# Performance work log

Hardware: AMD Instinct MI355X
Metric: run time of the kernel (lower is better)

Reference implementation:

```python
import jax, jax.numpy as jnp
import numpy as np
from jax import lax

FEAT_STRIDE = 16
SCALES = np.array([8, 16, 32], dtype=np.float64)
RATIOS = np.array([0.5, 1, 2], dtype=np.float64)
PRE_NMS_TOP_N = 6000
POST_NMS_TOP_N = 1000
NMS_THRESH = 0.7

# ---- anchor generation (numpy, static constants) ----

def _whctrs(a):
    w = a[2] - a[0] + 1.0
    h = a[3] - a[1] + 1.0
    return w, h, a[0] + 0.5 * (w - 1.0), a[1] + 0.5 * (h - 1.0)

def _mkanchors(ws, hs, xc, yc):
    return np.stack([xc - 0.5 * (ws - 1.0), yc - 0.5 * (hs - 1.0),
                     xc + 0.5 * (ws - 1.0), yc + 0.5 * (hs - 1.0)], axis=1)

def _ratio_enum(anchor, ratios):
    w, h, xc, yc = _whctrs(anchor)
    size = w * h
    ws = np.round(np.sqrt(size / ratios))
    hs = np.round(ws * ratios)
    return _mkanchors(ws, hs, xc, yc)

def _scale_enum(anchor, scales):
    w, h, xc, yc = _whctrs(anchor)
    return _mkanchors(w * scales, h * scales, xc, yc)

def generate_anchors(base_size=16):
    base = np.array([1, 1, base_size, base_size], dtype=np.float64) - 1.0
    ra = _ratio_enum(base, RATIOS)
    return np.vstack([_scale_enum(ra[i], SCALES) for i in range(ra.shape[0])]).astype(np.float32)


def setup_inputs() -> dict:
    key = jax.random.key(0)
    k1, k2 = jax.random.split(key)
    H, W, A = 76, 128, 9
    scores = jax.random.uniform(k1, (1, 2 * A, H, W), dtype=jnp.float32)
    bbox_delta = jax.random.normal(k2, (1, 4 * A, H, W), dtype=jnp.float32) * 0.1
    im_info = jnp.array([H * FEAT_STRIDE, W * FEAT_STRIDE, 1.0], dtype=jnp.float32)  # [h, w, scale]
    return {"scores": scores, "bbox_delta": bbox_delta, "im_info": im_info}


def reference(scores, bbox_delta, im_info):
    anchors = generate_anchors()            # [A, 4]
    A = anchors.shape[0]
    H, W = scores.shape[2], scores.shape[3]

    # grid of shifted anchors: [K*A, 4], anchor index varies fastest (matches permute layout)
    sx = np.arange(W) * FEAT_STRIDE
    sy = np.arange(H) * FEAT_STRIDE
    sx, sy = np.meshgrid(sx, sy)
    shifts = np.stack([sx.ravel(), sy.ravel(), sx.ravel(), sy.ravel()], axis=1).astype(np.float32)  # [K,4]
    all_anchors = jnp.asarray((anchors[None, :, :] + shifts[:, None, :]).reshape(-1, 4))  # [K*A,4]

    # foreground scores, NHWC flatten -> [K*A]
    fg = jnp.transpose(scores[0, A:], (1, 2, 0)).reshape(-1)
    # deltas, NHWC flatten -> [K*A, 4]
    deltas = jnp.transpose(bbox_delta[0], (1, 2, 0)).reshape(-1, 4)

    aw = all_anchors[:, 2] - all_anchors[:, 0] + 1.0
    ah = all_anchors[:, 3] - all_anchors[:, 1] + 1.0
    acx = all_anchors[:, 0] + 0.5 * aw
    acy = all_anchors[:, 1] + 0.5 * ah
    pcx = deltas[:, 0] * aw + acx
    pcy = deltas[:, 1] * ah + acy
    pw = jnp.exp(deltas[:, 2]) * aw
    ph = jnp.exp(deltas[:, 3]) * ah
    boxes = jnp.stack([pcx - 0.5 * pw, pcy - 0.5 * ph, pcx + 0.5 * pw, pcy + 0.5 * ph], axis=1)

    # clip_boxes to image
    xmax = im_info[1] - 1.0
    ymax = im_info[0] - 1.0
    boxes = jnp.stack([jnp.clip(boxes[:, 0], 0.0, xmax), jnp.clip(boxes[:, 1], 0.0, ymax),
                       jnp.clip(boxes[:, 2], 0.0, xmax), jnp.clip(boxes[:, 3], 0.0, ymax)], axis=1)

    # pre-NMS top-N by fg score
    top_scores, top_idx = lax.top_k(fg, PRE_NMS_TOP_N)
    props = boxes[top_idx]                  # [N, 4], sorted by score desc

    # pairwise IoU (+1 convention)
    x1, y1, x2, y2 = props[:, 0], props[:, 1], props[:, 2], props[:, 3]
    areas = (x2 - x1 + 1.0) * (y2 - y1 + 1.0)
    iw = jnp.clip(jnp.minimum(x2[:, None], x2[None, :]) - jnp.maximum(x1[:, None], x1[None, :]) + 1.0, 0.0)
    ih = jnp.clip(jnp.minimum(y2[:, None], y2[None, :]) - jnp.maximum(y1[:, None], y1[None, :]) + 1.0, 0.0)
    inter = iw * ih
    iou = inter / (areas[:, None] + areas[None, :] - inter)  # [N, N]

    # sequential greedy NMS over score-sorted boxes
    N = PRE_NMS_TOP_N
    later = jnp.arange(N)
    def body(i, keep):
        sup = (iou[i] > NMS_THRESH) & keep[i] & (later > i)
        return keep & ~sup
    keep = lax.fori_loop(0, N, body, jnp.ones((N,), dtype=bool))

    masked = jnp.where(keep, top_scores, -jnp.inf)
    _, sel = lax.top_k(masked, POST_NMS_TOP_N)
    return props[sel]                       # [POST_NMS_TOP_N, 4]
```

## Files before the change

### kernel.cpp

```cpp
#include <hip/hip_runtime.h>
#include <cstdint>

#define HH 76
#define WW 128
#define AA 9
#define HWH (HH * WW)
#define KK (HWH * AA)
#define NSEL 6000
#define NCH 94
#define NPAD (NCH * 64)
#define NOUT 1000
#define NMS_T 0.7
#define NTRI (NCH * (NCH + 1) / 2)
#define MASK_BLOCKS 1117
#define SELCAP 16384
#define BINCAP 2048
#define NBIN 16384

#define LBAR() asm volatile("s_waitcnt lgkmcnt(0)\n\ts_barrier" ::: "memory")

#define WS_HIST 0
#define WS_BINB 65536
#define WS_NACT 65540
#define WS_ACTIVE 65552
#define WS_BINSTART 98320
#define WS_SELKEYS 163856
#define WS_BOXES 294928
#define WS_MASK 391184

__device__ __constant__ float c_ax1[9] = {-84.f, -176.f, -360.f, -56.f, -120.f, -248.f, -36.f, -80.f, -168.f};
__device__ __constant__ float c_ay1[9] = {-40.f, -88.f, -184.f, -56.f, -120.f, -248.f, -80.f, -168.f, -344.f};
__device__ __constant__ float c_ax2[9] = {99.f, 191.f, 375.f, 71.f, 135.f, 263.f, 51.f, 95.f, 183.f};
__device__ __constant__ float c_ay2[9] = {55.f, 103.f, 199.f, 71.f, 135.f, 263.f, 95.f, 183.f, 359.f};

__device__ __forceinline__ unsigned score_key(float s) {
    unsigned u = __float_as_uint(s);
    return (u & 0x80000000u) ? ~u : (u | 0x80000000u);
}

__device__ __forceinline__ int key_bin(unsigned key) {
    int bi = (int)(key >> 16) - 0x8000;
    return bi < 0 ? 0 : (bi > NBIN - 1 ? NBIN - 1 : bi);
}

__device__ __forceinline__ unsigned long long chunk_scan_fix(unsigned long long col,
                                                             unsigned long long alive_in) {
    unsigned long long kept = alive_in;
    while (true) {
        unsigned long long sup = __ballot((int)((col & kept) != 0ull));
        unsigned long long kept2 = alive_in & ~sup;
        if (kept2 == kept) return kept;
        kept = kept2;
    }
}

__global__ __launch_bounds__(1024) void k_front1(const float* __restrict__ scores,
                                                 unsigned* __restrict__ histG,
                                                 unsigned* __restrict__ binB,
                                                 unsigned* __restrict__ binStart,
                                                 unsigned* __restrict__ activeList,
                                                 unsigned* __restrict__ nact,
                                                 unsigned long long* __restrict__ selKeys) {
    __shared__ unsigned hloc[NBIN];
    __shared__ unsigned seg[1024];
    __shared__ unsigned Bsh;
    int t = threadIdx.x;
    if (t == 0) *nact = 0;
#pragma unroll
    for (int k = 0; k < NBIN / 1024; ++k) hloc[t + k * 1024] = 0;
    __syncthreads();
    for (int g = t; g < KK / 4; g += 1024) {
        float4 v = ((const float4*)(scores + AA * HWH))[g];
        atomicAdd(&hloc[key_bin(score_key(v.x))], 1u);
        atomicAdd(&hloc[key_bin(score_key(v.y))], 1u);
        atomicAdd(&hloc[key_bin(score_key(v.z))], 1u);
        atomicAdd(&hloc[key_bin(score_key(v.w))], 1u);
    }
    __syncthreads();

    unsigned local[16];
    unsigned ssum = 0;
#pragma unroll
    for (int k = 0; k < 16; ++k) { local[k] = hloc[t * 16 + k]; ssum += local[k]; }
    seg[t] = ssum;
    __syncthreads();
    for (int off = 1; off < 1024; off <<= 1) {
        unsigned v = seg[t];
        unsigned add = (t + off < 1024) ? seg[t + off] : 0u;
        __syncthreads();
        seg[t] = v + add;
        __syncthreads();
    }
    unsigned above = (t + 1 < 1024) ? seg[t + 1] : 0u;
    if (above < NSEL && above + ssum >= NSEL) {
        unsigned acc = above;
#pragma unroll
        for (int b = 15; b >= 0; --b) {
            acc += local[b];
            if (acc >= NSEL) { Bsh = (unsigned)(t * 16 + b); *binB = Bsh; break; }
        }
    }
    __syncthreads();
    unsigned B = Bsh;
    if ((unsigned)(t * 16 + 15) >= B) {
        unsigned acc2 = above;
        for (int k = 15; k >= 0; --k) {
            unsigned bin = (unsigned)(t * 16 + k);
            if (bin < B) break;
            if (local[k] > 0) {
                binStart[bin] = acc2;
                histG[bin] = local[k];
                hloc[bin] = acc2;
                unsigned tick = atomicAdd(nact, 1u);
                if (tick < 8192) activeList[tick] = bin;
            }
            acc2 += local[k];
        }
    }
    __syncthreads();

    for (int g = t; g < KK / 4; g += 1024) {
        float4 v = ((const float4*)(scores + AA * HWH))[g];
        float sv[4] = {v.x, v.y, v.z, v.w};
#pragma unroll
        for (int k = 0; k < 4; ++k) {
            int j = g * 4 + k;
            unsigned key = score_key(sv[k]);
            unsigned bin = (unsigned)key_bin(key);
            if (bin >= B) {
                int a = j / HWH;
                int hw = j - a * HWH;
                unsigned i = (unsigned)(hw * AA + a);
                unsigned pos = atomicAdd(&hloc[bin], 1u);
                if (pos < SELCAP)
                    selKeys[pos] = ((unsigned long long)key << 32) | (unsigned)(~i);
            }
        }
    }
}

__global__ __launch_bounds__(256) void k_binsort(const unsigned* __restrict__ histG,
                                                 const unsigned* __restrict__ binStart,
                                                 const unsigned* __restrict__ activeList,
                                                 const unsigned* __restrict__ nact,
                                                 unsigned long long* __restrict__ selKeys,
                                                 const float* __restrict__ bbox,
                                                 const float* __restrict__ im_info,
                                                 float4* __restrict__ boxes) {
    __shared__ unsigned long long sk[BINCAP];
    int t = threadIdx.x;
    unsigned na = *nact;
    if (na > 8192) na = 8192;
    double xmax = (double)im_info[1] - 1.0, ymax = (double)im_info[0] - 1.0;
    for (unsigned aIdx = blockIdx.x; aIdx < na; aIdx += gridDim.x) {
        unsigned bin = activeList[aIdx];
        unsigned ntot = histG[bin];
        unsigned base = binStart[bin];
        unsigned n = ntot > BINCAP ? BINCAP : ntot;
        unsigned m = 64; while (m < n) m <<= 1;
        for (unsigned p = t; p < m; p += 256) sk[p] = (p < n) ? selKeys[base + p] : 0ull;
        __syncthreads();
        for (unsigned size = 2; size <= m; size <<= 1) {
            for (unsigned stride = size >> 1; stride > 0; stride >>= 1) {
                for (unsigned p = (unsigned)t; p < m / 2; p += 256) {
                    unsigned i = 2u * p - (p & (stride - 1u));
                    unsigned j = i + stride;
                    bool up = (i & size) != 0;
                    unsigned long long a = sk[i], b = sk[j];
                    bool doswap = up ? (a > b) : (a < b);
                    if (doswap) { sk[i] = b; sk[j] = a; }
                }
                __syncthreads();
            }
        }
        for (unsigned r = t; r < n; r += 256) {
            unsigned g = base + r;
            if (g >= NSEL) continue;
            unsigned i = ~(unsigned)(sk[r] & 0xFFFFFFFFull);
            int a = (int)(i % AA);
            int hw = (int)(i / AA);
            int h = hw >> 7, w = hw & 127;
            double sx = 16.0 * w, sy = 16.0 * h;
            double ax1 = (double)c_ax1[a] + sx, ay1 = (double)c_ay1[a] + sy;
            double ax2 = (double)c_ax2[a] + sx, ay2 = (double)c_ay2[a] + sy;
            double aw = ax2 - ax1 + 1.0, ah = ay2 - ay1 + 1.0;
            double acx = ax1 + 0.5 * aw, acy = ay1 + 0.5 * ah;
            int bse = h * WW + w;
            double d0 = (double)bbox[(4 * a + 0) * HWH + bse];
            double d1 = (double)bbox[(4 * a + 1) * HWH + bse];
            double d2 = (double)bbox[(4 * a + 2) * HWH + bse];
            double d3 = (double)bbox[(4 * a + 3) * HWH + bse];
            double pcx = d0 * aw + acx, pcy = d1 * ah + acy;
            double pw = exp(d2) * aw, ph = exp(d3) * ah;
            double x1 = fmin(fmax(pcx - 0.5 * pw, 0.0), xmax);
            double y1 = fmin(fmax(pcy - 0.5 * ph, 0.0), ymax);
            double x2 = fmin(fmax(pcx + 0.5 * pw, 0.0), xmax);
            double y2 = fmin(fmax(pcy + 0.5 * ph, 0.0), ymax);
            boxes[g] = make_float4((float)x1, (float)y1, (float)x2, (float)y2);
        }
        __syncthreads();
    }
}

__global__ __launch_bounds__(256) void k_mask(const float4* __restrict__ boxes,
                                              unsigned long long* __restrict__ supT) {
    __shared__ float4 cb[4][64];
    int wave = threadIdx.x >> 6, lane = threadIdx.x & 63;
    for (int L = blockIdx.x * 4 + wave; L < NTRI; L += MASK_BLOCKS * 4) {
        int rc = 0, rem = L;
        while (rem >= NCH - rc) { rem -= NCH - rc; rc++; }
        int cc = rc + rem;
        cb[wave][lane] = boxes[cc * 64 + lane];
        int gi = rc * 64 + lane;
        unsigned long long bits = 0ull;
        if (gi < NSEL) {
            float4 rb = boxes[gi];
            double rx1 = rb.x, ry1 = rb.y, rx2 = rb.z, ry2 = rb.w;
            double rarea = (rx2 - rx1 + 1.0) * (ry2 - ry1 + 1.0);
            for (int j = 0; j < 64; ++j) {
                int gj = cc * 64 + j;
                float4 c = cb[wave][j];
                double iw = fmin(rx2, (double)c.z) - fmax(rx1, (double)c.x) + 1.0;
                double ih = fmin(ry2, (double)c.w) - fmax(ry1, (double)c.y) + 1.0;
                if (gj > gi && gj < NSEL && iw > 0.0 && ih > 0.0) {
                    double inter = iw * ih;
                    double carea = ((double)c.z - (double)c.x + 1.0) * ((double)c.w - (double)c.y + 1.0);
                    double uni = rarea + carea - inter;
                    if (inter > NMS_T * uni) bits |= (1ull << j);
                }
            }
        }
        unsigned long long myword = 0ull;
        for (int j = 0; j < 64; ++j) {
            unsigned long long bal = __ballot((int)((bits >> j) & 1ull));
            if (lane == j) myword = bal;
        }
        supT[(size_t)rc * NPAD + cc * 64 + lane] = myword;
    }
}

__global__ __launch_bounds__(512, 1) void k_nms(const unsigned long long* __restrict__ supT,
                                                const float4* __restrict__ boxes,
                                                float4* __restrict__ out) {
    __shared__ unsigned long long colLds[NCH][64];
    __shared__ unsigned long long removed[NCH];
    __shared__ unsigned long long aliveArr[NCH];
    __shared__ int cstop;
    __shared__ unsigned scanBuf[8];
    int t = threadIdx.x;
    int wave = t >> 6, lane = t & 63;

    for (int c = wave; c < NCH; c += 8)
        colLds[c][lane] = supT[(size_t)c * NPAD + c * 64 + lane];
    for (int i = t; i < NCH; i += 512) removed[i] = (i == NCH - 1) ? 0xFFFF000000000000ull : 0ull;
    if (t == 0) cstop = -1;
    __syncthreads();
    if (wave == 0) __builtin_amdgcn_s_setprio(1);

    unsigned long long wAA = 0, wAB = 0;
    unsigned long long mA[8], mB[8];
#pragma unroll
    for (int q = 0; q < 8; ++q) { mA[q] = 0; mB[q] = 0; }
    if (wave == 0) wAA = supT[(size_t)0 * NPAD + 1 * 64 + lane];
    unsigned keptTot = 0;

    for (int c = 0; c < NCH; c += 2) {
        if (wave == 0) {
            if (c + 2 < NCH) wAB = supT[(size_t)(c + 1) * NPAD + (c + 2) * 64 + lane];
            unsigned long long alive_in = ~removed[c];
            unsigned long long alive = chunk_scan_fix(colLds[c][lane], alive_in);
            keptTot += (unsigned)__popcll(alive);
            if (lane == 0) {
                removed[c] = ~alive;
                aliveArr[c] = alive;
                if (keptTot >= NOUT) cstop = c;
            }
            if (c + 1 < NCH) {
                unsigned long long ball = __ballot((int)((wAA & alive) != 0ull));
                if (lane == 0 && ball) atomicOr(&removed[c + 1], ball);
            }
        } else {
            if (c + 2 < NCH) {
#pragma unroll
                for (int q = 0; q < 8; ++q) {
                    int cp = (wave - 1) + 7 * q;
                    mB[q] = (cp < c + 1) ? supT[(size_t)cp * NPAD + (c + 2) * 64 + lane] : 0ull;
                }
            }
            if (c + 1 < NCH) {
                unsigned long long acc = 0ull;
#pragma unroll
                for (int q = 0; q < 8; ++q) {
                    int cp = (wave - 1) + 7 * q;
                    if (cp < c) acc |= __ballot((int)((mA[q] & aliveArr[cp]) != 0ull));
                }
                for (int cp = (wave - 1) + 56; cp < c; cp += 7) {
                    unsigned long long wv = supT[(size_t)cp * NPAD + (c + 1) * 64 + lane];
                    acc |= __ballot((int)((wv & aliveArr[cp]) != 0ull));
                }
                if (lane == 0 && acc) atomicOr(&removed[c + 1], acc);
            }
        }
        LBAR();
        if (cstop >= 0) break;
        if (c + 1 >= NCH) break;

        if (wave == 0) {
            if (c + 3 < NCH) wAA = supT[(size_t)(c + 2) * NPAD + (c + 3) * 64 + lane];
            unsigned long long alive_in = ~removed[c + 1];
            unsigned long long alive = chunk_scan_fix(colLds[c + 1][lane], alive_in);
            keptTot += (unsigned)__popcll(alive);
            if (lane == 0) {
                removed[c + 1] = ~alive;
                aliveArr[c + 1] = alive;
                if (keptTot >= NOUT) cstop = c + 1;
            }
            if (c + 2 < NCH) {
                unsigned long long ball = __ballot((int)((wAB & alive) != 0ull));
                if (lane == 0 && ball) atomicOr(&removed[c + 2], ball);
            }
        } else {
            if (c + 3 < NCH) {
#pragma unroll
                for (int q = 0; q < 8; ++q) {
                    int cp = (wave - 1) + 7 * q;
                    mA[q] = (cp < c + 2) ? supT[(size_t)cp * NPAD + (c + 3) * 64 + lane] : 0ull;
                }
            }
            if (c + 2 < NCH) {
                unsigned long long acc = 0ull;
#pragma unroll
                for (int q = 0; q < 8; ++q) {
                    int cp = (wave - 1) + 7 * q;
                    if (cp < c + 1) acc |= __ballot((int)((mB[q] & aliveArr[cp]) != 0ull));
                }
                for (int cp = (wave - 1) + 56; cp < c + 1; cp += 7) {
                    unsigned long long wv = supT[(size_t)cp * NPAD + (c + 2) * 64 + lane];
                    acc |= __ballot((int)((wv & aliveArr[cp]) != 0ull));
                }
                if (lane == 0 && acc) atomicOr(&removed[c + 2], acc);
            }
        }
        LBAR();
        if (cstop >= 0) break;
    }
    if (wave == 0) __builtin_amdgcn_s_setprio(0);
    __syncthreads();

    int base = t * 12;
    unsigned cnt = 0, keepbits = 0;
    for (int q = 0; q < 12; ++q) {
        int i = base + q;
        if (i < NSEL) {
            bool kp = !((removed[i >> 6] >> (i & 63)) & 1ull);
            if (kp) { cnt++; keepbits |= (1u << q); }
        }
    }
    unsigned v = cnt;
#pragma unroll
    for (int off = 1; off < 64; off <<= 1) {
        unsigned u = (unsigned)__shfl_up((int)v, off, 64);
        if (lane >= off) v += u;
    }
    if (lane == 63) scanBuf[wave] = v;
    __syncthreads();
    unsigned waveOff = 0, NK = 0;
#pragma unroll
    for (int ww = 0; ww < 8; ++ww) {
        unsigned wv = scanBuf[ww];
        if (ww < wave) waveOff += wv;
        NK += wv;
    }
    unsigned incl = waveOff + v;
    unsigned kpos = incl - cnt;
    for (int q = 0; q < 12; ++q) {
        int i = base + q;
        if (i < NSEL) {
            bool kp = (keepbits >> q) & 1u;
            unsigned pos = kp ? kpos : (NK + (unsigned)i - kpos);
            if (kp) kpos++;
            if (pos < NOUT) out[pos] = boxes[i];
        }
    }
}

extern "C" void kernel_launch(void* const* d_in, const int* in_sizes, int n_in,
                              void* d_out, int out_size, void* d_ws, size_t ws_size,
                              hipStream_t stream) {
    const float* scores = (const float*)d_in[0];
    const float* bbox = (const float*)d_in[1];
    const float* im_info = (const float*)d_in[2];
    char* ws = (char*)d_ws;

    unsigned* histG = (unsigned*)(ws + WS_HIST);
    unsigned* binB = (unsigned*)(ws + WS_BINB);
    unsigned* nact = (unsigned*)(ws + WS_NACT);
    unsigned* activeList = (unsigned*)(ws + WS_ACTIVE);
    unsigned* binStart = (unsigned*)(ws + WS_BINSTART);
    unsigned long long* selKeys = (unsigned long long*)(ws + WS_SELKEYS);
    float4* boxes = (float4*)(ws + WS_BOXES);
    unsigned long long* supT = (unsigned long long*)(ws + WS_MASK);
    float4* out = (float4*)d_out;

    k_front1<<<1, 1024, 0, stream>>>(scores, histG, binB, binStart, activeList, nact, selKeys);
    k_binsort<<<64, 256, 0, stream>>>(histG, binStart, activeList, nact, selKeys, bbox, im_info, boxes);
    k_mask<<<MASK_BLOCKS, 256, 0, stream>>>(boxes, supT);
    k_nms<<<1, 512, 0, stream>>>(supT, boxes, out);
}
```

Measured before the change: 97.85 us.

## Fuse bin-sort and IoU mask kernels with a grid-wide atomic barrier

Merges the per-bin sort and box-decode kernel with the pairwise suppression-mask kernel into a single launch. The first 64 blocks sort bins and write boxes, then signal an atomic counter, and every block spins until that counter reaches 64 before computing mask tiles. This removes one kernel launch and its inter-kernel gap. In exchange it relies on all blocks being co-resident, and the larger shared buffer may lower occupancy in the mask phase.

```diff
diff --git a/kernel.cpp b/kernel.cpp
--- a/kernel.cpp
+++ b/kernel.cpp
@@ -12,7 +12,8 @@
 #define NOUT 1000
 #define NMS_T 0.7
 #define NTRI (NCH * (NCH + 1) / 2)
-#define MASK_BLOCKS 1117
+#define SM_BLOCKS 1117
+#define SORT_BLOCKS 64
 #define SELCAP 16384
 #define BINCAP 2048
 #define NBIN 16384
@@ -22,6 +23,7 @@
 #define WS_HIST 0
 #define WS_BINB 65536
 #define WS_NACT 65540
+#define WS_DONE 65544
 #define WS_ACTIVE 65552
 #define WS_BINSTART 98320
 #define WS_SELKEYS 163856
@@ -60,12 +62,13 @@
                                                  unsigned* __restrict__ binStart,
                                                  unsigned* __restrict__ activeList,
                                                  unsigned* __restrict__ nact,
+                                                 unsigned* __restrict__ doneCtr,
                                                  unsigned long long* __restrict__ selKeys) {
     __shared__ unsigned hloc[NBIN];
     __shared__ unsigned seg[1024];
     __shared__ unsigned Bsh;
     int t = threadIdx.x;
-    if (t == 0) *nact = 0;
+    if (t == 0) { *nact = 0; *doneCtr = 0; }
 #pragma unroll
     for (int k = 0; k < NBIN / 1024; ++k) hloc[t + k * 1024] = 0;
     __syncthreads();
@@ -139,78 +142,92 @@
     }
 }
 
-__global__ __launch_bounds__(256) void k_binsort(const unsigned* __restrict__ histG,
-                                                 const unsigned* __restrict__ binStart,
-                                                 const unsigned* __restrict__ activeList,
-                                                 const unsigned* __restrict__ nact,
-                                                 unsigned long long* __restrict__ selKeys,
-                                                 const float* __restrict__ bbox,
-                                                 const float* __restrict__ im_info,
-                                                 float4* __restrict__ boxes) {
-    __shared__ unsigned long long sk[BINCAP];
+__global__ __launch_bounds__(256) void k_sortmask(const unsigned* __restrict__ histG,
+                                                  const unsigned* __restrict__ binStart,
+                                                  const unsigned* __restrict__ activeList,
+                                                  const unsigned* __restrict__ nact,
+                                                  unsigned long long* __restrict__ selKeys,
+                                                  const float* __restrict__ bbox,
+                                                  const float* __restrict__ im_info,
+                                                  float4* __restrict__ boxes,
+                                                  unsigned* __restrict__ doneCtr,
+                                                  unsigned long long* __restrict__ supT) {
+    __shared__ __align__(16) unsigned long long shm[BINCAP];
     int t = threadIdx.x;
-    unsigned na = *nact;
-    if (na > 8192) na = 8192;
-    double xmax = (double)im_info[1] - 1.0, ymax = (double)im_info[0] - 1.0;
-    for (unsigned aIdx = blockIdx.x; aIdx < na; aIdx += gridDim.x) {
-        unsigned bin = activeList[aIdx];
-        unsigned ntot = histG[bin];
-        unsigned base = binStart[bin];
-        unsigned n = ntot > BINCAP ? BINCAP : ntot;
-        unsigned m = 64; while (m < n) m <<= 1;
-        for (unsigned p = t; p < m; p += 256) sk[p] = (p < n) ? selKeys[base + p] : 0ull;
+
+    if (blockIdx.x < SORT_BLOCKS) {
+        unsigned long long* sk = shm;
+        unsigned na = *nact;
+        if (na > 8192) na = 8192;
+        double xmax = (double)im_info[1] - 1.0, ymax = (double)im_info[0] - 1.0;
+        for (unsigned aIdx = blockIdx.x; aIdx < na; aIdx += SORT_BLOCKS) {
+            unsigned bin = activeList[aIdx];
+            unsigned ntot = histG[bin];
+            unsigned base = binStart[bin];
+            unsigned n = ntot > BINCAP ? BINCAP : ntot;
+            unsigned m = 64; while (m < n) m <<= 1;
+            for (unsigned p = t; p < m; p += 256) sk[p] = (p < n) ? selKeys[base + p] : 0ull;
+            __syncthreads();
+            for (unsigned size = 2; size <= m; size <<= 1) {
+                for (unsigned stride = size >> 1; stride > 0; stride >>= 1) {
+                    for (unsigned p = (unsigned)t; p < m / 2; p += 256) {
+                        unsigned i = 2u * p - (p & (stride - 1u));
+                        unsigned j = i + stride;
+                        bool up = (i & size) != 0;
+                        unsigned long long a = sk[i], b = sk[j];
+                        bool doswap = up ? (a > b) : (a < b);
+                        if (doswap) { sk[i] = b; sk[j] = a; }
+                    }
+                    __syncthreads();
+                }
+            }
+            for (unsigned r = t; r < n; r += 256) {
+                unsigned g = base + r;
+                if (g >= NSEL) continue;
+                unsigned i = ~(unsigned)(sk[r] & 0xFFFFFFFFull);
+                int a = (int)(i % AA);
+                int hw = (int)(i / AA);
+                int h = hw >> 7, w = hw & 127;
+                double sx = 16.0 * w, sy = 16.0 * h;
+                double ax1 = (double)c_ax1[a] + sx, ay1 = (double)c_ay1[a] + sy;
+                double ax2 = (double)c_ax2[a] + sx, ay2 = (double)c_ay2[a] + sy;
+                double aw = ax2 - ax1 + 1.0, ah = ay2 - ay1 + 1.0;
+                double acx = ax1 + 0.5 * aw, acy = ay1 + 0.5 * ah;
+                int bse = h * WW + w;
+                double d0 = (double)bbox[(4 * a + 0) * HWH + bse];
+                double d1 = (double)bbox[(4 * a + 1) * HWH + bse];
+                double d2 = (double)bbox[(4 * a + 2) * HWH + bse];
+                double d3 = (double)bbox[(4 * a + 3) * HWH + bse];
+                double pcx = d0 * aw + acx, pcy = d1 * ah + acy;
+                double pw = exp(d2) * aw, ph = exp(d3) * ah;
+                double x1 = fmin(fmax(pcx - 0.5 * pw, 0.0), xmax);
+                double y1 = fmin(fmax(pcy - 0.5 * ph, 0.0), ymax);
+                double x2 = fmin(fmax(pcx + 0.5 * pw, 0.0), xmax);
+                double y2 = fmin(fmax(pcy + 0.5 * ph, 0.0), ymax);
+                boxes[g] = make_float4((float)x1, (float)y1, (float)x2, (float)y2);
+            }
+            __syncthreads();
+        }
+        __threadfence();
         __syncthreads();
-        for (unsigned size = 2; size <= m; size <<= 1) {
-            for (unsigned stride = size >> 1; stride > 0; stride >>= 1) {
-                for (unsigned p = (unsigned)t; p < m / 2; p += 256) {
-                    unsigned i = 2u * p - (p & (stride - 1u));
-                    unsigned j = i + stride;
-                    bool up = (i & size) != 0;
-                    unsigned long long a = sk[i], b = sk[j];
-                    bool doswap = up ? (a > b) : (a < b);
-                    if (doswap) { sk[i] = b; sk[j] = a; }
-                }
-                __syncthreads();
-            }
-        }
-        for (unsigned r = t; r < n; r += 256) {
-            unsigned g = base + r;
-            if (g >= NSEL) continue;
-            unsigned i = ~(unsigned)(sk[r] & 0xFFFFFFFFull);
-            int a = (int)(i % AA);
-            int hw = (int)(i / AA);
-            int h = hw >> 7, w = hw & 127;
-            double sx = 16.0 * w, sy = 16.0 * h;
-            double ax1 = (double)c_ax1[a] + sx, ay1 = (double)c_ay1[a] + sy;
-            double ax2 = (double)c_ax2[a] + sx, ay2 = (double)c_ay2[a] + sy;
-            double aw = ax2 - ax1 + 1.0, ah = ay2 - ay1 + 1.0;
-            double acx = ax1 + 0.5 * aw, acy = ay1 + 0.5 * ah;
-            int bse = h * WW + w;
-            double d0 = (double)bbox[(4 * a + 0) * HWH + bse];
-            double d1 = (double)bbox[(4 * a + 1) * HWH + bse];
-            double d2 = (double)bbox[(4 * a + 2) * HWH + bse];
-            double d3 = (double)bbox[(4 * a + 3) * HWH + bse];
-            double pcx = d0 * aw + acx, pcy = d1 * ah + acy;
-            double pw = exp(d2) * aw, ph = exp(d3) * ah;
-            double x1 = fmin(fmax(pcx - 0.5 * pw, 0.0), xmax);
-            double y1 = fmin(fmax(pcy - 0.5 * ph, 0.0), ymax);
-            double x2 = fmin(fmax(pcx + 0.5 * pw, 0.0), xmax);
-            double y2 = fmin(fmax(pcy + 0.5 * ph, 0.0), ymax);
-            boxes[g] = make_float4((float)x1, (float)y1, (float)x2, (float)y2);
-        }
-        __syncthreads();
-    }
-}
-
-__global__ __launch_bounds__(256) void k_mask(const float4* __restrict__ boxes,
-                                              unsigned long long* __restrict__ supT) {
-    __shared__ float4 cb[4][64];
-    int wave = threadIdx.x >> 6, lane = threadIdx.x & 63;
-    for (int L = blockIdx.x * 4 + wave; L < NTRI; L += MASK_BLOCKS * 4) {
+        if (t == 0) __hip_atomic_fetch_add(doneCtr, 1u, __ATOMIC_ACQ_REL, __HIP_MEMORY_SCOPE_AGENT);
+    }
+
+    if (t == 0) {
+        while (__hip_atomic_load(doneCtr, __ATOMIC_ACQUIRE, __HIP_MEMORY_SCOPE_AGENT) <
+               (unsigned)SORT_BLOCKS)
+            __builtin_amdgcn_s_sleep(1);
+    }
+    __syncthreads();
+    __threadfence();
+
+    float4* cb = (float4*)shm;
+    int wave = t >> 6, lane = t & 63;
+    for (int L = blockIdx.x * 4 + wave; L < NTRI; L += SM_BLOCKS * 4) {
         int rc = 0, rem = L;
         while (rem >= NCH - rc) { rem -= NCH - rc; rc++; }
         int cc = rc + rem;
-        cb[wave][lane] = boxes[cc * 64 + lane];
+        cb[wave * 64 + lane] = boxes[cc * 64 + lane];
         int gi = rc * 64 + lane;
         unsigned long long bits = 0ull;
         if (gi < NSEL) {
@@ -219,7 +236,7 @@
             double rarea = (rx2 - rx1 + 1.0) * (ry2 - ry1 + 1.0);
             for (int j = 0; j < 64; ++j) {
                 int gj = cc * 64 + j;
-                float4 c = cb[wave][j];
+                float4 c = cb[wave * 64 + j];
                 double iw = fmin(rx2, (double)c.z) - fmax(rx1, (double)c.x) + 1.0;
                 double ih = fmin(ry2, (double)c.w) - fmax(ry1, (double)c.y) + 1.0;
                 if (gj > gi && gj < NSEL && iw > 0.0 && ih > 0.0) {
@@ -395,6 +412,7 @@
     unsigned* histG = (unsigned*)(ws + WS_HIST);
     unsigned* binB = (unsigned*)(ws + WS_BINB);
     unsigned* nact = (unsigned*)(ws + WS_NACT);
+    unsigned* doneCtr = (unsigned*)(ws + WS_DONE);
     unsigned* activeList = (unsigned*)(ws + WS_ACTIVE);
     unsigned* binStart = (unsigned*)(ws + WS_BINSTART);
     unsigned long long* selKeys = (unsigned long long*)(ws + WS_SELKEYS);
@@ -402,8 +420,8 @@
     unsigned long long* supT = (unsigned long long*)(ws + WS_MASK);
     float4* out = (float4*)d_out;
 
-    k_front1<<<1, 1024, 0, stream>>>(scores, histG, binB, binStart, activeList, nact, selKeys);
-    k_binsort<<<64, 256, 0, stream>>>(histG, binStart, activeList, nact, selKeys, bbox, im_info, boxes);
-    k_mask<<<MASK_BLOCKS, 256, 0, stream>>>(boxes, supT);
+    k_front1<<<1, 1024, 0, stream>>>(scores, histG, binB, binStart, activeList, nact, doneCtr, selKeys);
+    k_sortmask<<<SM_BLOCKS, 256, 0, stream>>>(histG, binStart, activeList, nact, selKeys,
+                                              bbox, im_info, boxes, doneCtr, supT);
     k_nms<<<1, 512, 0, stream>>>(supT, boxes, out);
 }
```

New measurement: 260.6 us. +166.4%, slower.

## Fuse per-bin sort and box decode into front kernel using rank sort

Applied to the files above, without the earlier changes.

Removes the separate k_binsort launch and runs the per-bin sorting and box decoding inside the single-block k_front1 kernel. Each of the 16 waves takes bins in turn and places every key by rank counting in LDS instead of a bitonic sort. Bins larger than 512 entries are deferred to a block-wide rank-sort pass. This saves a kernel launch and the bitonic barrier rounds, but all of the decode and sort work now runs on one workgroup instead of 64 blocks.

```diff
diff --git a/kernel.cpp b/kernel.cpp
--- a/kernel.cpp
+++ b/kernel.cpp
@@ -14,7 +14,6 @@
 #define NTRI (NCH * (NCH + 1) / 2)
 #define MASK_BLOCKS 1117
 #define SELCAP 16384
-#define BINCAP 2048
 #define NBIN 16384
 
 #define LBAR() asm volatile("s_waitcnt lgkmcnt(0)\n\ts_barrier" ::: "memory")
@@ -54,18 +53,49 @@
     }
 }
 
+__device__ __forceinline__ void decode_box(unsigned i, double xmax, double ymax,
+                                           const float* __restrict__ bbox,
+                                           float4* __restrict__ boxes, unsigned g) {
+    int a = (int)(i % AA);
+    int hw = (int)(i / AA);
+    int h = hw >> 7, w = hw & 127;
+    double sx = 16.0 * w, sy = 16.0 * h;
+    double ax1 = (double)c_ax1[a] + sx, ay1 = (double)c_ay1[a] + sy;
+    double ax2 = (double)c_ax2[a] + sx, ay2 = (double)c_ay2[a] + sy;
+    double aw = ax2 - ax1 + 1.0, ah = ay2 - ay1 + 1.0;
+    double acx = ax1 + 0.5 * aw, acy = ay1 + 0.5 * ah;
+    int bse = h * WW + w;
+    double d0 = (double)bbox[(4 * a + 0) * HWH + bse];
+    double d1 = (double)bbox[(4 * a + 1) * HWH + bse];
+    double d2 = (double)bbox[(4 * a + 2) * HWH + bse];
+    double d3 = (double)bbox[(4 * a + 3) * HWH + bse];
+    double pcx = d0 * aw + acx, pcy = d1 * ah + acy;
+    double pw = exp(d2) * aw, ph = exp(d3) * ah;
+    double x1 = fmin(fmax(pcx - 0.5 * pw, 0.0), xmax);
+    double y1 = fmin(fmax(pcy - 0.5 * ph, 0.0), ymax);
+    double x2 = fmin(fmax(pcx + 0.5 * pw, 0.0), xmax);
+    double y2 = fmin(fmax(pcy + 0.5 * ph, 0.0), ymax);
+    boxes[g] = make_float4((float)x1, (float)y1, (float)x2, (float)y2);
+}
+
 __global__ __launch_bounds__(1024) void k_front1(const float* __restrict__ scores,
+                                                 const float* __restrict__ bbox,
+                                                 const float* __restrict__ im_info,
                                                  unsigned* __restrict__ histG,
                                                  unsigned* __restrict__ binB,
                                                  unsigned* __restrict__ binStart,
                                                  unsigned* __restrict__ activeList,
                                                  unsigned* __restrict__ nact,
-                                                 unsigned long long* __restrict__ selKeys) {
-    __shared__ unsigned hloc[NBIN];
-    __shared__ unsigned seg[1024];
+                                                 unsigned long long* __restrict__ selKeys,
+                                                 float4* __restrict__ boxes) {
+    __shared__ __align__(16) unsigned char smemBuf[NBIN * 4 + 4096];
     __shared__ unsigned Bsh;
+    __shared__ unsigned bigList[64];
+    __shared__ unsigned nbig;
+    unsigned* hloc = (unsigned*)smemBuf;
+    unsigned* seg = (unsigned*)(smemBuf + NBIN * 4);
     int t = threadIdx.x;
-    if (t == 0) *nact = 0;
+    if (t == 0) { *nact = 0; nbig = 0; }
 #pragma unroll
     for (int k = 0; k < NBIN / 1024; ++k) hloc[t + k * 1024] = 0;
     __syncthreads();
@@ -137,66 +167,52 @@
             }
         }
     }
-}
-
-__global__ __launch_bounds__(256) void k_binsort(const unsigned* __restrict__ histG,
-                                                 const unsigned* __restrict__ binStart,
-                                                 const unsigned* __restrict__ activeList,
-                                                 const unsigned* __restrict__ nact,
-                                                 unsigned long long* __restrict__ selKeys,
-                                                 const float* __restrict__ bbox,
-                                                 const float* __restrict__ im_info,
-                                                 float4* __restrict__ boxes) {
-    __shared__ unsigned long long sk[BINCAP];
-    int t = threadIdx.x;
+    __syncthreads();
+
+    double xmax = (double)im_info[1] - 1.0, ymax = (double)im_info[0] - 1.0;
     unsigned na = *nact;
     if (na > 8192) na = 8192;
-    double xmax = (double)im_info[1] - 1.0, ymax = (double)im_info[0] - 1.0;
-    for (unsigned aIdx = blockIdx.x; aIdx < na; aIdx += gridDim.x) {
+    int wave = t >> 6, lane = t & 63;
+    unsigned long long* skbAll = (unsigned long long*)smemBuf;
+    unsigned long long* skb = skbAll + wave * 512;
+    for (unsigned aIdx = (unsigned)wave; aIdx < na; aIdx += 16) {
         unsigned bin = activeList[aIdx];
-        unsigned ntot = histG[bin];
+        unsigned n = histG[bin];
         unsigned base = binStart[bin];
-        unsigned n = ntot > BINCAP ? BINCAP : ntot;
-        unsigned m = 64; while (m < n) m <<= 1;
-        for (unsigned p = t; p < m; p += 256) sk[p] = (p < n) ? selKeys[base + p] : 0ull;
+        if (n > 512) {
+            if (lane == 0) {
+                unsigned p = atomicAdd(&nbig, 1u);
+                if (p < 64) bigList[p] = aIdx;
+            }
+            continue;
+        }
+        for (unsigned p = lane; p < n; p += 64) skb[p] = selKeys[base + p];
+        asm volatile("s_waitcnt lgkmcnt(0)" ::: "memory");
+        for (unsigned r = lane; r < n; r += 64) {
+            unsigned long long key = skb[r];
+            unsigned rank = 0;
+            for (unsigned j = 0; j < n; ++j) rank += (skb[j] > key) ? 1u : 0u;
+            unsigned g = base + rank;
+            if (g < NSEL) decode_box(~(unsigned)(key & 0xFFFFFFFFull), xmax, ymax, bbox, boxes, g);
+        }
+    }
+    __syncthreads();
+    unsigned nb = nbig;
+    if (nb > 64) nb = 64;
+    for (unsigned b = 0; b < nb; ++b) {
+        unsigned aIdx = bigList[b];
+        unsigned bin = activeList[aIdx];
+        unsigned n = histG[bin];
+        if (n > 8192) n = 8192;
+        unsigned base = binStart[bin];
+        for (unsigned p = t; p < n; p += 1024) skbAll[p] = selKeys[base + p];
         __syncthreads();
-        for (unsigned size = 2; size <= m; size <<= 1) {
-            for (unsigned stride = size >> 1; stride > 0; stride >>= 1) {
-                for (unsigned p = (unsigned)t; p < m / 2; p += 256) {
-                    unsigned i = 2u * p - (p & (stride - 1u));
-                    unsigned j = i + stride;
-                    bool up = (i & size) != 0;
-                    unsigned long long a = sk[i], b = sk[j];
-                    bool doswap = up ? (a > b) : (a < b);
-                    if (doswap) { sk[i] = b; sk[j] = a; }
-                }
-                __syncthreads();
-            }
-        }
-        for (unsigned r = t; r < n; r += 256) {
-            unsigned g = base + r;
-            if (g >= NSEL) continue;
-            unsigned i = ~(unsigned)(sk[r] & 0xFFFFFFFFull);
-            int a = (int)(i % AA);
-            int hw = (int)(i / AA);
-            int h = hw >> 7, w = hw & 127;
-            double sx = 16.0 * w, sy = 16.0 * h;
-            double ax1 = (double)c_ax1[a] + sx, ay1 = (double)c_ay1[a] + sy;
-            double ax2 = (double)c_ax2[a] + sx, ay2 = (double)c_ay2[a] + sy;
-            double aw = ax2 - ax1 + 1.0, ah = ay2 - ay1 + 1.0;
-            double acx = ax1 + 0.5 * aw, acy = ay1 + 0.5 * ah;
-            int bse = h * WW + w;
-            double d0 = (double)bbox[(4 * a + 0) * HWH + bse];
-            double d1 = (double)bbox[(4 * a + 1) * HWH + bse];
-            double d2 = (double)bbox[(4 * a + 2) * HWH + bse];
-            double d3 = (double)bbox[(4 * a + 3) * HWH + bse];
-            double pcx = d0 * aw + acx, pcy = d1 * ah + acy;
-            double pw = exp(d2) * aw, ph = exp(d3) * ah;
-            double x1 = fmin(fmax(pcx - 0.5 * pw, 0.0), xmax);
-            double y1 = fmin(fmax(pcy - 0.5 * ph, 0.0), ymax);
-            double x2 = fmin(fmax(pcx + 0.5 * pw, 0.0), xmax);
-            double y2 = fmin(fmax(pcy + 0.5 * ph, 0.0), ymax);
-            boxes[g] = make_float4((float)x1, (float)y1, (float)x2, (float)y2);
+        for (unsigned r = t; r < n; r += 1024) {
+            unsigned long long key = skbAll[r];
+            unsigned rank = 0;
+            for (unsigned j = 0; j < n; ++j) rank += (skbAll[j] > key) ? 1u : 0u;
+            unsigned g = base + rank;
+            if (g < NSEL) decode_box(~(unsigned)(key & 0xFFFFFFFFull), xmax, ymax, bbox, boxes, g);
         }
         __syncthreads();
     }
@@ -402,8 +418,8 @@
     unsigned long long* supT = (unsigned long long*)(ws + WS_MASK);
     float4* out = (float4*)d_out;
 
-    k_front1<<<1, 1024, 0, stream>>>(scores, histG, binB, binStart, activeList, nact, selKeys);
-    k_binsort<<<64, 256, 0, stream>>>(histG, binStart, activeList, nact, selKeys, bbox, im_info, boxes);
+    k_front1<<<1, 1024, 0, stream>>>(scores, bbox, im_info, histG, binB, binStart,
+                                     activeList, nact, selKeys, boxes);
     k_mask<<<MASK_BLOCKS, 256, 0, stream>>>(boxes, supT);
     k_nms<<<1, 512, 0, stream>>>(supT, boxes, out);
 }
```

After: 294.0 us. 3x slower.

## Process two NMS chunks per barrier in the block-serial greedy NMS loop

Applied to the files above, without the earlier changes.

The NMS loop now handles an even/odd pair of 64-box chunks per barrier step instead of one chunk per barrier. Wave 0 resolves both chunks in sequence, using register-held suppression words for the intra-pair and next-pair dependencies. The other waves compute contributions to chunks e+2 and e+3 from earlier chunks and prefetch two chunks ahead. This halves the number of block-wide barriers on the serial critical path, at the cost of more registers and more work per step.

```diff
diff --git a/kernel.cpp b/kernel.cpp
--- a/kernel.cpp
+++ b/kernel.cpp
@@ -18,6 +18,7 @@
 #define NBIN 16384
 
 #define LBAR() asm volatile("s_waitcnt lgkmcnt(0)\n\ts_barrier" ::: "memory")
+#define LWAIT() asm volatile("s_waitcnt lgkmcnt(0)" ::: "memory")
 
 #define WS_HIST 0
 #define WS_BINB 65536
@@ -257,89 +258,97 @@
     __syncthreads();
     if (wave == 0) __builtin_amdgcn_s_setprio(1);
 
-    unsigned long long wAA = 0, wAB = 0;
+    unsigned long long w_eo = 0, w_e2 = 0, w_e3 = 0, w_o2 = 0, w_o3 = 0;
     unsigned long long mA[8], mB[8];
 #pragma unroll
     for (int q = 0; q < 8; ++q) { mA[q] = 0; mB[q] = 0; }
-    if (wave == 0) wAA = supT[(size_t)0 * NPAD + 1 * 64 + lane];
+    if (wave == 0) {
+        w_eo = supT[(size_t)0 * NPAD + 1 * 64 + lane];
+        w_e2 = supT[(size_t)0 * NPAD + 2 * 64 + lane];
+        w_e3 = supT[(size_t)0 * NPAD + 3 * 64 + lane];
+        w_o2 = supT[(size_t)1 * NPAD + 2 * 64 + lane];
+        w_o3 = supT[(size_t)1 * NPAD + 3 * 64 + lane];
+    }
     unsigned keptTot = 0;
 
-    for (int c = 0; c < NCH; c += 2) {
+    for (int e = 0; e < NCH; e += 2) {
+        int o = e + 1;
         if (wave == 0) {
-            if (c + 2 < NCH) wAB = supT[(size_t)(c + 1) * NPAD + (c + 2) * 64 + lane];
-            unsigned long long alive_in = ~removed[c];
-            unsigned long long alive = chunk_scan_fix(colLds[c][lane], alive_in);
-            keptTot += (unsigned)__popcll(alive);
+            unsigned long long nw_eo = 0, nw_e2 = 0, nw_e3 = 0, nw_o2 = 0, nw_o3 = 0;
+            if (e + 2 < NCH) {
+                int e2 = e + 2, o2 = e + 3;
+                nw_eo = supT[(size_t)e2 * NPAD + o2 * 64 + lane];
+                nw_e2 = (e2 + 2 < NCH) ? supT[(size_t)e2 * NPAD + (e2 + 2) * 64 + lane] : 0ull;
+                nw_e3 = (e2 + 3 < NCH) ? supT[(size_t)e2 * NPAD + (e2 + 3) * 64 + lane] : 0ull;
+                nw_o2 = (e2 + 2 < NCH) ? supT[(size_t)o2 * NPAD + (e2 + 2) * 64 + lane] : 0ull;
+                nw_o3 = (e2 + 3 < NCH) ? supT[(size_t)o2 * NPAD + (e2 + 3) * 64 + lane] : 0ull;
+            }
+            unsigned long long alive_e = chunk_scan_fix(colLds[e][lane], ~removed[e]);
+            keptTot += (unsigned)__popcll(alive_e);
             if (lane == 0) {
-                removed[c] = ~alive;
-                aliveArr[c] = alive;
-                if (keptTot >= NOUT) cstop = c;
-            }
-            if (c + 1 < NCH) {
-                unsigned long long ball = __ballot((int)((wAA & alive) != 0ull));
-                if (lane == 0 && ball) atomicOr(&removed[c + 1], ball);
-            }
+                removed[e] = ~alive_e;
+                aliveArr[e] = alive_e;
+                if (keptTot >= NOUT && cstop < 0) cstop = e;
+            }
+            {
+                unsigned long long ball = __ballot((int)((w_eo & alive_e) != 0ull));
+                if (lane == 0 && ball) atomicOr(&removed[o], ball);
+            }
+            LWAIT();
+            unsigned long long alive_o = chunk_scan_fix(colLds[o][lane], ~removed[o]);
+            keptTot += (unsigned)__popcll(alive_o);
+            if (lane == 0) {
+                removed[o] = ~alive_o;
+                aliveArr[o] = alive_o;
+                if (keptTot >= NOUT && cstop < 0) cstop = o;
+            }
+            if (e + 2 < NCH) {
+                unsigned long long b1 = __ballot((int)((w_e2 & alive_e) != 0ull)) |
+                                        __ballot((int)((w_o2 & alive_o) != 0ull));
+                if (lane == 0 && b1) atomicOr(&removed[e + 2], b1);
+            }
+            if (e + 3 < NCH) {
+                unsigned long long b2 = __ballot((int)((w_e3 & alive_e) != 0ull)) |
+                                        __ballot((int)((w_o3 & alive_o) != 0ull));
+                if (lane == 0 && b2) atomicOr(&removed[e + 3], b2);
+            }
+            w_eo = nw_eo; w_e2 = nw_e2; w_e3 = nw_e3; w_o2 = nw_o2; w_o3 = nw_o3;
         } else {
-            if (c + 2 < NCH) {
+            unsigned long long nA[8], nB[8];
+#pragma unroll
+            for (int q = 0; q < 8; ++q) {
+                int cp = (wave - 1) + 7 * q;
+                nA[q] = (e + 4 < NCH && cp < e + 2) ? supT[(size_t)cp * NPAD + (e + 4) * 64 + lane] : 0ull;
+                nB[q] = (e + 5 < NCH && cp < e + 2) ? supT[(size_t)cp * NPAD + (e + 5) * 64 + lane] : 0ull;
+            }
+            if (e + 2 < NCH) {
+                unsigned long long acc = 0ull;
 #pragma unroll
                 for (int q = 0; q < 8; ++q) {
                     int cp = (wave - 1) + 7 * q;
-                    mB[q] = (cp < c + 1) ? supT[(size_t)cp * NPAD + (c + 2) * 64 + lane] : 0ull;
-                }
-            }
-            if (c + 1 < NCH) {
+                    if (cp < e) acc |= __ballot((int)((mA[q] & aliveArr[cp]) != 0ull));
+                }
+                for (int cp = (wave - 1) + 56; cp < e; cp += 7) {
+                    unsigned long long wv = supT[(size_t)cp * NPAD + (e + 2) * 64 + lane];
+                    acc |= __ballot((int)((wv & aliveArr[cp]) != 0ull));
+                }
+                if (lane == 0 && acc) atomicOr(&removed[e + 2], acc);
+            }
+            if (e + 3 < NCH) {
                 unsigned long long acc = 0ull;
 #pragma unroll
                 for (int q = 0; q < 8; ++q) {
                     int cp = (wave - 1) + 7 * q;
-                    if (cp < c) acc |= __ballot((int)((mA[q] & aliveArr[cp]) != 0ull));
-                }
-                for (int cp = (wave - 1) + 56; cp < c; cp += 7) {
-                    unsigned long long wv = supT[(size_t)cp * NPAD + (c + 1) * 64 + lane];
+                    if (cp < e) acc |= __ballot((int)((mB[q] & aliveArr[cp]) != 0ull));
+                }
+                for (int cp = (wave - 1) + 56; cp < e; cp += 7) {
+                    unsigned long long wv = supT[(size_t)cp * NPAD + (e + 3) * 64 + lane];
                     acc |= __ballot((int)((wv & aliveArr[cp]) != 0ull));
                 }
-                if (lane == 0 && acc) atomicOr(&removed[c + 1], acc);
-            }
-        }
-        LBAR();
-        if (cstop >= 0) break;
-        if (c + 1 >= NCH) break;
-
-        if (wave == 0) {
-            if (c + 3 < NCH) wAA = supT[(size_t)(c + 2) * NPAD + (c + 3) * 64 + lane];
-            unsigned long long alive_in = ~removed[c + 1];
-            unsigned long long alive = chunk_scan_fix(colLds[c + 1][lane], alive_in);
-            keptTot += (unsigned)__popcll(alive);
-            if (lane == 0) {
-                removed[c + 1] = ~alive;
-                aliveArr[c + 1] = alive;
-                if (keptTot >= NOUT) cstop = c + 1;
-            }
-            if (c + 2 < NCH) {
-                unsigned long long ball = __ballot((int)((wAB & alive) != 0ull));
-                if (lane == 0 && ball) atomicOr(&removed[c + 2], ball);
-            }
-        } else {
-            if (c + 3 < NCH) {
-#pragma unroll
-                for (int q = 0; q < 8; ++q) {
-                    int cp = (wave - 1) + 7 * q;
-                    mA[q] = (cp < c + 2) ? supT[(size_t)cp * NPAD + (c + 3) * 64 + lane] : 0ull;
-                }
-            }
-            if (c + 2 < NCH) {
-                unsigned long long acc = 0ull;
-#pragma unroll
-                for (int q = 0; q < 8; ++q) {
-                    int cp = (wave - 1) + 7 * q;
-                    if (cp < c + 1) acc |= __ballot((int)((mB[q] & aliveArr[cp]) != 0ull));
-                }
-                for (int cp = (wave - 1) + 56; cp < c + 1; cp += 7) {
-                    unsigned long long wv = supT[(size_t)cp * NPAD + (c + 2) * 64 + lane];
-                    acc |= __ballot((int)((wv & aliveArr[cp]) != 0ull));
-                }
-                if (lane == 0 && acc) atomicOr(&removed[c + 2], acc);
-            }
+                if (lane == 0 && acc) atomicOr(&removed[e + 3], acc);
+            }
+#pragma unroll
+            for (int q = 0; q < 8; ++q) { mA[q] = nA[q]; mB[q] = nB[q]; }
         }
         LBAR();
         if (cstop >= 0) break;
```

Result: faster. 95.35 us (-2.6%).
